# Kernel optimization log

Hardware: AMD Instinct MI355X
Metric: run time of the kernel (lower is better)

## Reference

```python
import jax, jax.numpy as jnp
import numpy as np

N_NODES = 50000
D_IN = 128
HIDDEN = 128
UNITS_DENSE = 256
N_EDGES = 600000
N_PRED = 200000
N_SEL = 300000


def setup_inputs() -> dict:
    key = jax.random.key(0)
    ks = jax.random.split(key, 12)
    node_state = jax.random.normal(ks[0], (N_NODES, D_IN), jnp.float32)
    edge_index = jax.random.randint(ks[1], (2, N_EDGES), 0, N_NODES, jnp.int32)
    out_edges = jax.random.randint(ks[2], (2, N_PRED), 0, N_NODES, jnp.int32)
    set_idx = jnp.sort(jax.random.randint(ks[3], (N_SEL,), 0, 2 * N_PRED, jnp.int32))
    # Glorot-ish scaled weights
    W1 = jax.random.normal(ks[4], (D_IN, HIDDEN), jnp.float32) / np.float32(np.sqrt(D_IN))
    b1 = jnp.zeros((HIDDEN,), jnp.float32)
    W2 = jax.random.normal(ks[5], (HIDDEN, HIDDEN), jnp.float32) / np.float32(np.sqrt(HIDDEN))
    b2 = jnp.zeros((HIDDEN,), jnp.float32)
    dense_W = jax.random.normal(ks[6], (2 * 0 + HIDDEN, UNITS_DENSE), jnp.float32) / np.float32(np.sqrt(HIDDEN))
    dense_b = jnp.zeros((UNITS_DENSE,), jnp.float32)
    out_W = jax.random.normal(ks[7], (UNITS_DENSE, 2), jnp.float32) / np.float32(np.sqrt(UNITS_DENSE))
    out_b = jnp.zeros((2,), jnp.float32)
    return {
        "node_state": node_state, "edge_index": edge_index, "out_edges": out_edges,
        "set_idx": set_idx, "W1": W1, "b1": b1, "W2": W2, "b2": b2,
        "dense_W": dense_W, "dense_b": dense_b, "out_W": out_W, "out_b": out_b,
    }


def _graph_conv(h, src, dst, W, b):
    """DGL GraphConv, norm='both', no activation: D_in^{-1/2} A D_out^{-1/2} H W + b."""
    n = h.shape[0]
    ones = jnp.ones(src.shape[0], h.dtype)
    deg_out = jnp.clip(jax.ops.segment_sum(ones, src, num_segments=n), 1.0)  # [N]
    deg_in = jnp.clip(jax.ops.segment_sum(ones, dst, num_segments=n), 1.0)   # [N]
    h = (h * jax.lax.rsqrt(deg_out)[:, None]) @ W                            # [N, H]
    agg = jax.ops.segment_sum(h[src], dst, num_segments=n)                   # [N, H]
    return agg * jax.lax.rsqrt(deg_in)[:, None] + b


def reference(node_state, edge_index, out_edges, set_idx,
              W1, b1, W2, b2, dense_W, dense_b, out_W, out_b):
    src, dst = edge_index[0], edge_index[1]
    h = _graph_conv(node_state, src, dst, W1, b1)
    h = _graph_conv(h, src, dst, W2, b2)
    # concat along axis=0 as in the original: [2*E_pred, H]
    edge_state = jnp.concatenate([h[out_edges[0]], h[out_edges[1]]], axis=0)
    # boolean_mask replaced by equivalent gather of selected (True) rows
    edge_state_set = edge_state[set_idx]                                      # [N_SEL, H]
    hidden = jax.nn.relu(edge_state_set @ dense_W + dense_b)
    return jax.nn.softmax(hidden @ out_W + out_b, axis=-1)
```

## Files before the change

kernel.cpp:

```cpp
#include <hip/hip_runtime.h>

#define NN 50000
#define DD 128
#define NE 600000
#define NP 200000
#define NS 300000
#define NU 256
#define NBH 64
#define EPB 9375
#define NW 12500
#define NB64 782

typedef __attribute__((ext_vector_type(8))) short short8;
typedef __attribute__((ext_vector_type(4))) float floatx4;

__device__ inline float bf2f(unsigned int u16) {
    unsigned int x = u16 << 16;
    float f; __builtin_memcpy(&f, &x, 4); return f;
}
__device__ inline unsigned short f2bf(float f) {
    unsigned int x; __builtin_memcpy(&x, &f, 4);
    unsigned int lsb = (x >> 16) & 1u;
    x += 0x7fffu + lsb;
    return (unsigned short)(x >> 16);
}

__global__ __launch_bounds__(256) void k_hist(const int* __restrict__ ei,
                                              unsigned int* __restrict__ P) {
    __shared__ unsigned int hw[NW];
    int b = blockIdx.x, half = blockIdx.y, tid = threadIdx.x;
    for (int w = tid; w < NW; w += 256) hw[w] = 0;
    __syncthreads();
    const int* src = ei + (size_t)half * NE;
    int e0 = b * EPB, e1 = min(e0 + EPB, NE);
    for (int e = e0 + tid; e < e1; e += 256) {
        int s = src[e];
        atomicAdd(&hw[s >> 2], 1u << ((s & 3) * 8));
    }
    __syncthreads();
    unsigned int* Pb = P + ((size_t)half * NBH + b) * NW;
    for (int w = tid; w < NW; w += 256) Pb[w] = hw[w];
}

__global__ void k_reduce(const unsigned int* __restrict__ P, int* __restrict__ deg_in,
                         float* __restrict__ r) {
    int w = blockIdx.x * 256 + threadIdx.x;
    if (w >= 2 * NW) return;
    int half = (w >= NW);
    int wl = w - half * NW;
    const unsigned int* Ph = P + (size_t)half * NBH * NW + wl;
    int c0 = 0, c1 = 0, c2 = 0, c3 = 0;
    for (int b = 0; b < NBH; ++b) {
        unsigned int v = Ph[(size_t)b * NW];
        c0 += v & 0xff; c1 += (v >> 8) & 0xff; c2 += (v >> 16) & 0xff; c3 += v >> 24;
    }
    int nb = wl * 4;
    if (half) {
        int4 d = {c0, c1, c2, c3};
        *(int4*)(deg_in + nb) = d;
    }
    float4 rr = {rsqrtf((float)max(c0, 1)), rsqrtf((float)max(c1, 1)),
                 rsqrtf((float)max(c2, 1)), rsqrtf((float)max(c3, 1))};
    *(float4*)(r + (size_t)half * NN + nb) = rr;
}

__global__ __launch_bounds__(1024) void k_scan(const int* __restrict__ deg_in,
                                               int* __restrict__ row_ptr) {
    __shared__ int wsum[16];
    __shared__ int woff[16];
    __shared__ int carry_s;
    __shared__ int total_s;
    int tid = threadIdx.x, lane = tid & 63, w = tid >> 6;
    if (tid == 0) carry_s = 0;
    __syncthreads();
    for (int wb = 0; wb < NW; wb += 1024) {
        int i4 = wb + tid;
        int4 v = {0, 0, 0, 0};
        if (i4 < NW) v = *(const int4*)(deg_in + i4 * 4);
        int t0 = v.x, t1 = t0 + v.y, t2 = t1 + v.z, tot = t2 + v.w;
        int x = tot;
#pragma unroll
        for (int off = 1; off < 64; off <<= 1) {
            int y = __shfl_up(x, off);
            if (lane >= off) x += y;
        }
        if (lane == 63) wsum[w] = x;
        __syncthreads();
        if (w == 0 && lane < 16) {
            int s = wsum[lane];
            int xs = s;
#pragma unroll
            for (int off = 1; off < 16; off <<= 1) {
                int y = __shfl_up(xs, off);
                if (lane >= off) xs += y;
            }
            woff[lane] = xs - s;
            if (lane == 15) total_s = xs;
        }
        __syncthreads();
        if (i4 < NW) {
            int base = carry_s + woff[w] + x - tot;
            int4 o = {base, base + t0, base + t1, base + t2};
            *(int4*)(row_ptr + i4 * 4) = o;
        }
        __syncthreads();
        if (tid == 0) carry_s += total_s;
        __syncthreads();
    }
    if (tid == 0) row_ptr[NN] = carry_s;
}

__global__ void k_colscan(const unsigned int* __restrict__ Pin, const int* __restrict__ row_ptr,
                          int* __restrict__ basetab) {
    int n = blockIdx.x * 256 + threadIdx.x;
    if (n >= NN) return;
    int wl = n >> 2, sh = (n & 3) * 8;
    int run = row_ptr[n];
    for (int b = 0; b < NBH; ++b) {
        basetab[(size_t)b * NN + n] = run;
        run += (Pin[(size_t)b * NW + wl] >> sh) & 0xff;
    }
}

__global__ __launch_bounds__(256) void k_bucket2(const int* __restrict__ ei,
                                                 const int* __restrict__ basetab,
                                                 int* __restrict__ col) {
    __shared__ unsigned int cw[NW];
    int b = blockIdx.x, tid = threadIdx.x;
    for (int w = tid; w < NW; w += 256) cw[w] = 0;
    __syncthreads();
    const int* bt = basetab + (size_t)b * NN;
    int e0 = b * EPB, e1 = min(e0 + EPB, NE);
    for (int e = e0 + tid; e < e1; e += 256) {
        int s = ei[e], d = ei[NE + e];
        int sh = (d & 3) * 8;
        unsigned int old = atomicAdd(&cw[d >> 2], 1u << sh);
        int local = (old >> sh) & 0xff;
        col[bt[d] + local] = s;
    }
}

__global__ void k_castW(const float* __restrict__ W1, const float* __restrict__ W2,
                        const float* __restrict__ dW, unsigned short* __restrict__ BT1,
                        unsigned short* __restrict__ BT2, unsigned short* __restrict__ BTd) {
    int t = blockIdx.x * 256 + threadIdx.x;
    if (t < 16384) {
        int r = t >> 7, c = t & 127;
        BT1[c * 128 + r] = f2bf(W1[t]);
    } else if (t < 32768) {
        int t2 = t - 16384;
        int r = t2 >> 7, c = t2 & 127;
        BT2[c * 128 + r] = f2bf(W2[t2]);
    } else if (t < 65536) {
        int t2 = t - 32768;
        int r = t2 >> 8, c = t2 & 255;
        BTd[c * 128 + r] = f2bf(dW[t2]);
    }
}

template <bool ABF>
__global__ __launch_bounds__(256) void k_gemm_bf(const void* __restrict__ Ap,
                                                 const float* __restrict__ rs,
                                                 const unsigned short* __restrict__ BT,
                                                 unsigned short* __restrict__ Cm) {
    __shared__ unsigned short As[64][136];
    __shared__ unsigned short Bs[128][136];
    int tid = threadIdx.x, lane = tid & 63, wave = tid >> 6;
    int quad = lane >> 4, l16 = lane & 15;
    int row0 = blockIdx.x * 64;

    if (ABF) {
        const unsigned short* A = (const unsigned short*)Ap;
#pragma unroll
        for (int p = 0; p < 4; ++p) {
            int fid = tid + p * 256;
            int r = fid >> 4, c = fid & 15;
            int gr = row0 + r; if (gr > NN - 1) gr = NN - 1;
            *(uint4*)&As[r][c * 8] = *(const uint4*)(A + (size_t)gr * DD + c * 8);
        }
    } else {
        const float* A = (const float*)Ap;
#pragma unroll
        for (int p = 0; p < 8; ++p) {
            int fid = tid + p * 256;
            int r = fid >> 5, c = fid & 31;
            int gr = row0 + r; if (gr > NN - 1) gr = NN - 1;
            float4 v = *(const float4*)(A + (size_t)gr * DD + c * 4);
            ushort4 u;
            u.x = f2bf(v.x); u.y = f2bf(v.y); u.z = f2bf(v.z); u.w = f2bf(v.w);
            *(ushort4*)&As[r][c * 4] = u;
        }
    }
#pragma unroll
    for (int p = 0; p < 8; ++p) {
        int fid = tid + p * 256;
        int r = fid >> 4, c = fid & 15;
        *(uint4*)&Bs[r][c * 8] = *(const uint4*)(BT + (size_t)r * DD + c * 8);
    }
    __syncthreads();

    short8 af[4];
#pragma unroll
    for (int ks = 0; ks < 4; ++ks)
        af[ks] = *(const short8*)&As[wave * 16 + l16][ks * 32 + quad * 8];
    floatx4 acc[8];
#pragma unroll
    for (int nt = 0; nt < 8; ++nt) acc[nt] = (floatx4){0.f, 0.f, 0.f, 0.f};
#pragma unroll
    for (int ks = 0; ks < 4; ++ks) {
#pragma unroll
        for (int nt = 0; nt < 8; ++nt) {
            short8 bf = *(const short8*)&Bs[nt * 16 + l16][ks * 32 + quad * 8];
            acc[nt] = __builtin_amdgcn_mfma_f32_16x16x32_bf16(af[ks], bf, acc[nt], 0, 0, 0);
        }
    }
    int rbase = row0 + wave * 16 + quad * 4;
#pragma unroll
    for (int r = 0; r < 4; ++r) {
        int gr = rbase + r;
        if (gr < NN) {
            float s = rs[gr];
#pragma unroll
            for (int nt = 0; nt < 8; ++nt)
                Cm[(size_t)gr * DD + nt * 16 + l16] = f2bf(acc[nt][r] * s);
        }
    }
}

__global__ __launch_bounds__(256) void k_aggregate(const unsigned short* __restrict__ T,
                                                   const int* __restrict__ row_ptr,
                                                   const int* __restrict__ col,
                                                   const float* __restrict__ r_in,
                                                   const float* __restrict__ b,
                                                   unsigned short* __restrict__ H) {
    int wave = threadIdx.x >> 6, lane = threadIdx.x & 63;
    int sub = lane >> 4, l16 = lane & 15;
    int node = blockIdx.x * 16 + wave * 4 + sub;
    if (node >= NN) return;
    int beg = row_ptr[node], end = row_ptr[node + 1];
    float a0 = 0.f, a1 = 0.f, a2 = 0.f, a3 = 0.f, a4 = 0.f, a5 = 0.f, a6 = 0.f, a7 = 0.f;
    for (int base = beg; base < end; base += 16) {
        int m = end - base; if (m > 16) m = 16;
        int myidx = (l16 < m) ? col[base + l16] : 0;
        int j = 0;
        for (; j + 2 <= m; j += 2) {
            int s0 = __shfl(myidx, (sub << 4) | j);
            int s1 = __shfl(myidx, (sub << 4) | (j + 1));
            uint4 v0 = *(const uint4*)(T + (size_t)s0 * DD + l16 * 8);
            uint4 v1 = *(const uint4*)(T + (size_t)s1 * DD + l16 * 8);
            a0 += bf2f(v0.x & 0xffff) + bf2f(v1.x & 0xffff);
            a1 += bf2f(v0.x >> 16)    + bf2f(v1.x >> 16);
            a2 += bf2f(v0.y & 0xffff) + bf2f(v1.y & 0xffff);
            a3 += bf2f(v0.y >> 16)    + bf2f(v1.y >> 16);
            a4 += bf2f(v0.z & 0xffff) + bf2f(v1.z & 0xffff);
            a5 += bf2f(v0.z >> 16)    + bf2f(v1.z >> 16);
            a6 += bf2f(v0.w & 0xffff) + bf2f(v1.w & 0xffff);
            a7 += bf2f(v0.w >> 16)    + bf2f(v1.w >> 16);
        }
        if (j < m) {
            int s0 = __shfl(myidx, (sub << 4) | j);
            uint4 v0 = *(const uint4*)(T + (size_t)s0 * DD + l16 * 8);
            a0 += bf2f(v0.x & 0xffff); a1 += bf2f(v0.x >> 16);
            a2 += bf2f(v0.y & 0xffff); a3 += bf2f(v0.y >> 16);
            a4 += bf2f(v0.z & 0xffff); a5 += bf2f(v0.z >> 16);
            a6 += bf2f(v0.w & 0xffff); a7 += bf2f(v0.w >> 16);
        }
    }
    float rv = r_in[node];
    float4 bl = *(const float4*)(b + l16 * 8);
    float4 bh = *(const float4*)(b + l16 * 8 + 4);
    uint4 w;
    w.x = (unsigned int)f2bf(a0 * rv + bl.x) | ((unsigned int)f2bf(a1 * rv + bl.y) << 16);
    w.y = (unsigned int)f2bf(a2 * rv + bl.z) | ((unsigned int)f2bf(a3 * rv + bl.w) << 16);
    w.z = (unsigned int)f2bf(a4 * rv + bh.x) | ((unsigned int)f2bf(a5 * rv + bh.y) << 16);
    w.w = (unsigned int)f2bf(a6 * rv + bh.z) | ((unsigned int)f2bf(a7 * rv + bh.w) << 16);
    *(uint4*)(H + (size_t)node * DD + l16 * 8) = w;
}

__global__ __launch_bounds__(256) void k_mlp_mfma(const unsigned short* __restrict__ H2,
                                                  const unsigned short* __restrict__ BTd,
                                                  const float* __restrict__ db,
                                                  const float* __restrict__ oW,
                                                  const float* __restrict__ ob,
                                                  float* __restrict__ P) {
    __shared__ unsigned short As[64][136];
    __shared__ unsigned short Bs[128][136];
    int tid = threadIdx.x, lane = tid & 63, wave = tid >> 6;
    int quad = lane >> 4, l16 = lane & 15;
    int row0 = blockIdx.x * 64;
#pragma unroll
    for (int p = 0; p < 4; ++p) {
        int fid = tid + p * 256;
        int r = fid >> 4, c = fid & 15;
        int gr = row0 + r; if (gr > NN - 1) gr = NN - 1;
        *(uint4*)&As[r][c * 8] = *(const uint4*)(H2 + (size_t)gr * DD + c * 8);
    }
    short8 af[4];
    floatx4 acc[16];
#pragma unroll
    for (int i = 0; i < 16; ++i) acc[i] = (floatx4){0.f, 0.f, 0.f, 0.f};

    for (int ch = 0; ch < 2; ++ch) {
        __syncthreads();
#pragma unroll
        for (int p = 0; p < 8; ++p) {
            int fid = tid + p * 256;
            int r = fid >> 4, c = fid & 15;
            *(uint4*)&Bs[r][c * 8] = *(const uint4*)(BTd + (size_t)(ch * 128 + r) * DD + c * 8);
        }
        __syncthreads();
        if (ch == 0) {
#pragma unroll
            for (int ks = 0; ks < 4; ++ks)
                af[ks] = *(const short8*)&As[wave * 16 + l16][ks * 32 + quad * 8];
        }
#pragma unroll
        for (int ks = 0; ks < 4; ++ks) {
#pragma unroll
            for (int nt = 0; nt < 8; ++nt) {
                short8 bf = *(const short8*)&Bs[nt * 16 + l16][ks * 32 + quad * 8];
                acc[ch * 8 + nt] =
                    __builtin_amdgcn_mfma_f32_16x16x32_bf16(af[ks], bf, acc[ch * 8 + nt], 0, 0, 0);
            }
        }
    }
    int rbase = row0 + wave * 16 + quad * 4;
#pragma unroll
    for (int r = 0; r < 4; ++r) {
        float p0 = 0.f, p1 = 0.f;
#pragma unroll
        for (int ch = 0; ch < 2; ++ch) {
#pragma unroll
            for (int nt = 0; nt < 8; ++nt) {
                int colc = ch * 128 + nt * 16 + l16;
                float h = acc[ch * 8 + nt][r] + db[colc];
                h = fmaxf(h, 0.f);
                p0 += h * oW[2 * colc];
                p1 += h * oW[2 * colc + 1];
            }
        }
#pragma unroll
        for (int m = 8; m >= 1; m >>= 1) {
            p0 += __shfl_xor(p0, m, 16);
            p1 += __shfl_xor(p1, m, 16);
        }
        if (l16 == 0) {
            int gr = rbase + r;
            if (gr < NN) {
                float l0 = p0 + ob[0], l1 = p1 + ob[1];
                float mx = fmaxf(l0, l1);
                float e0 = __expf(l0 - mx), e1 = __expf(l1 - mx);
                float inv = 1.f / (e0 + e1);
                float2 pr = {e0 * inv, e1 * inv};
                *(float2*)(P + 2 * gr) = pr;
            }
        }
    }
}

__global__ void k_gather(const int* __restrict__ sidx, const int* __restrict__ oe,
                         const float* __restrict__ P, float* __restrict__ out) {
    int i = blockIdx.x * 256 + threadIdx.x;
    if (i >= NS) return;
    int node = oe[sidx[i]];
    float2 v = *(const float2*)(P + 2 * node);
    *(float2*)(out + 2 * i) = v;
}

extern "C" void kernel_launch(void* const* d_in, const int* in_sizes, int n_in,
                              void* d_out, int out_size, void* d_ws, size_t ws_size,
                              hipStream_t stream) {
    const float* node_state = (const float*)d_in[0];
    const int* ei   = (const int*)d_in[1];
    const int* oe   = (const int*)d_in[2];
    const int* sidx = (const int*)d_in[3];
    const float* W1 = (const float*)d_in[4];
    const float* b1 = (const float*)d_in[5];
    const float* W2 = (const float*)d_in[6];
    const float* b2 = (const float*)d_in[7];
    const float* dW = (const float*)d_in[8];
    const float* db = (const float*)d_in[9];
    const float* oW = (const float*)d_in[10];
    const float* ob = (const float*)d_in[11];
    float* out = (float*)d_out;

    char* ws = (char*)d_ws;
    size_t off = 0;
    auto carve = [&](size_t bytes) -> char* {
        char* p = ws + off;
        off = (off + bytes + 255) & ~(size_t)255;
        return p;
    };
    int*   deg_in  = (int*)carve((size_t)NN * 4);
    float* r       = (float*)carve((size_t)2 * NN * 4);
    int*   row_ptr = (int*)carve((size_t)(NN + 1) * 4);
    int*   col     = (int*)carve((size_t)NE * 4);
    unsigned int* P_hist = (unsigned int*)carve((size_t)2 * NBH * NW * 4);
    int*   basetab = (int*)carve((size_t)NBH * NN * 4);
    unsigned short* t   = (unsigned short*)carve((size_t)NN * DD * 2);
    unsigned short* h   = (unsigned short*)carve((size_t)NN * DD * 2);
    unsigned short* BT1 = (unsigned short*)carve((size_t)DD * DD * 2);
    unsigned short* BT2 = (unsigned short*)carve((size_t)DD * DD * 2);
    unsigned short* BTd = (unsigned short*)carve((size_t)DD * NU * 2);
    float* P = (float*)t;

    float* r_out = r;
    float* r_in  = r + NN;

    k_hist<<<dim3(NBH, 2), 256, 0, stream>>>(ei, P_hist);
    k_reduce<<<(2 * NW + 255) / 256, 256, 0, stream>>>(P_hist, deg_in, r);
    k_scan<<<1, 1024, 0, stream>>>(deg_in, row_ptr);
    k_colscan<<<(NN + 255) / 256, 256, 0, stream>>>(P_hist + (size_t)NBH * NW, row_ptr, basetab);
    k_bucket2<<<NBH, 256, 0, stream>>>(ei, basetab, col);

    k_castW<<<256, 256, 0, stream>>>(W1, W2, dW, BT1, BT2, BTd);

    k_gemm_bf<false><<<NB64, 256, 0, stream>>>(node_state, r_out, BT1, t);
    k_aggregate<<<(NN + 15) / 16, 256, 0, stream>>>(t, row_ptr, col, r_in, b1, h);

    k_gemm_bf<true><<<NB64, 256, 0, stream>>>(h, r_out, BT2, t);
    k_aggregate<<<(NN + 15) / 16, 256, 0, stream>>>(t, row_ptr, col, r_in, b2, h);

    k_mlp_mfma<<<NB64, 256, 0, stream>>>(h, BTd, db, oW, ob, P);
    k_gather<<<(NS + 255) / 256, 256, 0, stream>>>(sidx, oe, P, out);
}
```

Measured before the change: 266.9 us.

## Fuse CSR build and weight cast into one cooperative kernel with grid syncs

Result: slower. 416.2 us (+55.9%).

```diff
diff --git a/kernel.cpp b/kernel.cpp
--- a/kernel.cpp
+++ b/kernel.cpp
@@ -1,4 +1,7 @@
 #include <hip/hip_runtime.h>
+#include <hip/hip_cooperative_groups.h>
+
+namespace cg = cooperative_groups;
 
 #define NN 50000
 #define DD 128
@@ -6,8 +9,8 @@
 #define NP 200000
 #define NS 300000
 #define NU 256
-#define NBH 64
-#define EPB 9375
+#define NBH 128
+#define EPB 4688
 #define NW 12500
 #define NB64 782
 
@@ -25,136 +28,122 @@
     return (unsigned short)(x >> 16);
 }
 
-__global__ __launch_bounds__(256) void k_hist(const int* __restrict__ ei,
-                                              unsigned int* __restrict__ P) {
+__global__ __launch_bounds__(256) void k_csr_coop(
+    const int* __restrict__ ei,
+    const float* __restrict__ W1, const float* __restrict__ W2, const float* __restrict__ dW,
+    unsigned short* __restrict__ BT1, unsigned short* __restrict__ BT2,
+    unsigned short* __restrict__ BTd,
+    unsigned int* __restrict__ P_hist, int* __restrict__ deg_in, float* __restrict__ r,
+    int* __restrict__ row_ptr, int* __restrict__ basetab, int* __restrict__ col,
+    int* __restrict__ blocksum, int* __restrict__ blockoff)
+{
     __shared__ unsigned int hw[NW];
-    int b = blockIdx.x, half = blockIdx.y, tid = threadIdx.x;
+    cg::grid_group grid = cg::this_grid();
+    int b = blockIdx.x, tid = threadIdx.x, lane = tid & 63;
+
     for (int w = tid; w < NW; w += 256) hw[w] = 0;
     __syncthreads();
-    const int* src = ei + (size_t)half * NE;
-    int e0 = b * EPB, e1 = min(e0 + EPB, NE);
+    int chunk = b & 127;
+    const int* eptr = ei + (b < 128 ? NE : 0);
+    int e0 = chunk * EPB, e1 = min(e0 + EPB, NE);
     for (int e = e0 + tid; e < e1; e += 256) {
-        int s = src[e];
-        atomicAdd(&hw[s >> 2], 1u << ((s & 3) * 8));
+        int v = eptr[e];
+        atomicAdd(&hw[v >> 2], 1u << ((v & 3) * 8));
     }
     __syncthreads();
-    unsigned int* Pb = P + ((size_t)half * NBH + b) * NW;
-    for (int w = tid; w < NW; w += 256) Pb[w] = hw[w];
-}
-
-__global__ void k_reduce(const unsigned int* __restrict__ P, int* __restrict__ deg_in,
-                         float* __restrict__ r) {
-    int w = blockIdx.x * 256 + threadIdx.x;
-    if (w >= 2 * NW) return;
-    int half = (w >= NW);
-    int wl = w - half * NW;
-    const unsigned int* Ph = P + (size_t)half * NBH * NW + wl;
-    int c0 = 0, c1 = 0, c2 = 0, c3 = 0;
-    for (int b = 0; b < NBH; ++b) {
-        unsigned int v = Ph[(size_t)b * NW];
-        c0 += v & 0xff; c1 += (v >> 8) & 0xff; c2 += (v >> 16) & 0xff; c3 += v >> 24;
-    }
-    int nb = wl * 4;
-    if (half) {
-        int4 d = {c0, c1, c2, c3};
-        *(int4*)(deg_in + nb) = d;
-    }
-    float4 rr = {rsqrtf((float)max(c0, 1)), rsqrtf((float)max(c1, 1)),
-                 rsqrtf((float)max(c2, 1)), rsqrtf((float)max(c3, 1))};
-    *(float4*)(r + (size_t)half * NN + nb) = rr;
-}
-
-__global__ __launch_bounds__(1024) void k_scan(const int* __restrict__ deg_in,
-                                               int* __restrict__ row_ptr) {
-    __shared__ int wsum[16];
-    __shared__ int woff[16];
-    __shared__ int carry_s;
-    __shared__ int total_s;
-    int tid = threadIdx.x, lane = tid & 63, w = tid >> 6;
-    if (tid == 0) carry_s = 0;
+    {
+        unsigned int* Pb = P_hist + (size_t)b * NW;
+        for (int w = tid; w < NW; w += 256) Pb[w] = hw[w];
+    }
+    grid.sync();
+
+    int gid = b * 256 + tid;
+    if (gid < 2 * NW) {
+        int half = gid >= NW;
+        int wl = gid - half * NW;
+        const unsigned int* Ph = P_hist + (size_t)(half ? 128 : 0) * NW + wl;
+        int c0 = 0, c1 = 0, c2 = 0, c3 = 0;
+        for (int b2 = 0; b2 < 128; ++b2) {
+            unsigned int v = Ph[(size_t)b2 * NW];
+            c0 += v & 0xff; c1 += (v >> 8) & 0xff; c2 += (v >> 16) & 0xff; c3 += v >> 24;
+        }
+        int nb4 = wl * 4;
+        if (!half) { int4 d4 = {c0, c1, c2, c3}; *(int4*)(deg_in + nb4) = d4; }
+        float4 rr = {rsqrtf((float)max(c0, 1)), rsqrtf((float)max(c1, 1)),
+                     rsqrtf((float)max(c2, 1)), rsqrtf((float)max(c3, 1))};
+        *(float4*)(r + (half ? 0 : NN) + nb4) = rr;
+    }
+    {
+        int t = gid;
+        if (t < 16384) { int rr = t >> 7, cc = t & 127; BT1[cc * 128 + rr] = f2bf(W1[t]); }
+        else if (t < 32768) { int t2 = t - 16384; int rr = t2 >> 7, cc = t2 & 127; BT2[cc * 128 + rr] = f2bf(W2[t2]); }
+        else { int t2 = t - 32768; int rr = t2 >> 8, cc = t2 & 255; BTd[cc * 128 + rr] = f2bf(dW[t2]); }
+    }
+    grid.sync();
+
+    int w49 = b * 49 + tid;
+    bool valid = (tid < 49) && (w49 < NW);
+    int4 v4 = {0, 0, 0, 0};
+    if (valid) v4 = *(const int4*)(deg_in + w49 * 4);
+    if (tid < 64) {
+        int s = v4.x + v4.y + v4.z + v4.w;
+        int x = s;
+#pragma unroll
+        for (int off = 1; off < 64; off <<= 1) { int y = __shfl_up(x, off); if (lane >= off) x += y; }
+        hw[tid] = (unsigned int)(x - s);
+        if (lane == 63) blocksum[b] = x;
+    }
+    grid.sync();
+
+    if (b == 0 && tid < 64) {
+        int s0 = blocksum[tid * 4], s1 = blocksum[tid * 4 + 1];
+        int s2 = blocksum[tid * 4 + 2], s3 = blocksum[tid * 4 + 3];
+        int tot = s0 + s1 + s2 + s3;
+        int x = tot;
+#pragma unroll
+        for (int off = 1; off < 64; off <<= 1) { int y = __shfl_up(x, off); if (lane >= off) x += y; }
+        int base0 = x - tot;
+        blockoff[tid * 4]     = base0;
+        blockoff[tid * 4 + 1] = base0 + s0;
+        blockoff[tid * 4 + 2] = base0 + s0 + s1;
+        blockoff[tid * 4 + 3] = base0 + s0 + s1 + s2;
+    }
+    grid.sync();
+
+    int bo = blockoff[b];
+    if (valid) {
+        int base = bo + (int)hw[tid];
+        int4 o = {base, base + v4.x, base + v4.x + v4.y, base + v4.x + v4.y + v4.z};
+        *(int4*)(row_ptr + w49 * 4) = o;
+        hw[256 + tid * 4]     = (unsigned int)o.x;
+        hw[256 + tid * 4 + 1] = (unsigned int)o.y;
+        hw[256 + tid * 4 + 2] = (unsigned int)o.z;
+        hw[256 + tid * 4 + 3] = (unsigned int)o.w;
+    }
+    if (b == 0 && tid == 0) row_ptr[NN] = NE;
     __syncthreads();
-    for (int wb = 0; wb < NW; wb += 1024) {
-        int i4 = wb + tid;
-        int4 v = {0, 0, 0, 0};
-        if (i4 < NW) v = *(const int4*)(deg_in + i4 * 4);
-        int t0 = v.x, t1 = t0 + v.y, t2 = t1 + v.z, tot = t2 + v.w;
-        int x = tot;
-#pragma unroll
-        for (int off = 1; off < 64; off <<= 1) {
-            int y = __shfl_up(x, off);
-            if (lane >= off) x += y;
-        }
-        if (lane == 63) wsum[w] = x;
-        __syncthreads();
-        if (w == 0 && lane < 16) {
-            int s = wsum[lane];
-            int xs = s;
-#pragma unroll
-            for (int off = 1; off < 16; off <<= 1) {
-                int y = __shfl_up(xs, off);
-                if (lane >= off) xs += y;
-            }
-            woff[lane] = xs - s;
-            if (lane == 15) total_s = xs;
-        }
-        __syncthreads();
-        if (i4 < NW) {
-            int base = carry_s + woff[w] + x - tot;
-            int4 o = {base, base + t0, base + t1, base + t2};
-            *(int4*)(row_ptr + i4 * 4) = o;
-        }
-        __syncthreads();
-        if (tid == 0) carry_s += total_s;
-        __syncthreads();
-    }
-    if (tid == 0) row_ptr[NN] = carry_s;
-}
-
-__global__ void k_colscan(const unsigned int* __restrict__ Pin, const int* __restrict__ row_ptr,
-                          int* __restrict__ basetab) {
-    int n = blockIdx.x * 256 + threadIdx.x;
-    if (n >= NN) return;
-    int wl = n >> 2, sh = (n & 3) * 8;
-    int run = row_ptr[n];
-    for (int b = 0; b < NBH; ++b) {
-        basetab[(size_t)b * NN + n] = run;
-        run += (Pin[(size_t)b * NW + wl] >> sh) & 0xff;
-    }
-}
-
-__global__ __launch_bounds__(256) void k_bucket2(const int* __restrict__ ei,
-                                                 const int* __restrict__ basetab,
-                                                 int* __restrict__ col) {
-    __shared__ unsigned int cw[NW];
-    int b = blockIdx.x, tid = threadIdx.x;
-    for (int w = tid; w < NW; w += 256) cw[w] = 0;
+
+    int n = b * 196 + tid;
+    if (tid < 196 && n < NN) {
+        int run = (int)hw[256 + tid];
+        int wl = n >> 2, sh = (n & 3) * 8;
+        for (int b2 = 0; b2 < 128; ++b2) {
+            basetab[(size_t)b2 * NN + n] = run;
+            run += (P_hist[(size_t)b2 * NW + wl] >> sh) & 0xff;
+        }
+    }
+    grid.sync();
+
+    if (b >= 128) return;
+    for (int w = tid; w < NW; w += 256) hw[w] = 0;
     __syncthreads();
     const int* bt = basetab + (size_t)b * NN;
-    int e0 = b * EPB, e1 = min(e0 + EPB, NE);
     for (int e = e0 + tid; e < e1; e += 256) {
         int s = ei[e], d = ei[NE + e];
         int sh = (d & 3) * 8;
-        unsigned int old = atomicAdd(&cw[d >> 2], 1u << sh);
+        unsigned int old = atomicAdd(&hw[d >> 2], 1u << sh);
         int local = (old >> sh) & 0xff;
         col[bt[d] + local] = s;
-    }
-}
-
-__global__ void k_castW(const float* __restrict__ W1, const float* __restrict__ W2,
-                        const float* __restrict__ dW, unsigned short* __restrict__ BT1,
-                        unsigned short* __restrict__ BT2, unsigned short* __restrict__ BTd) {
-    int t = blockIdx.x * 256 + threadIdx.x;
-    if (t < 16384) {
-        int r = t >> 7, c = t & 127;
-        BT1[c * 128 + r] = f2bf(W1[t]);
-    } else if (t < 32768) {
-        int t2 = t - 16384;
-        int r = t2 >> 7, c = t2 & 127;
-        BT2[c * 128 + r] = f2bf(W2[t2]);
-    } else if (t < 65536) {
-        int t2 = t - 32768;
-        int r = t2 >> 8, c = t2 & 255;
-        BTd[c * 128 + r] = f2bf(dW[t2]);
     }
 }
 
@@ -243,21 +232,25 @@
         int m = end - base; if (m > 16) m = 16;
         int myidx = (l16 < m) ? col[base + l16] : 0;
         int j = 0;
-        for (; j + 2 <= m; j += 2) {
+        for (; j + 4 <= m; j += 4) {
             int s0 = __shfl(myidx, (sub << 4) | j);
             int s1 = __shfl(myidx, (sub << 4) | (j + 1));
+            int s2 = __shfl(myidx, (sub << 4) | (j + 2));
+            int s3 = __shfl(myidx, (sub << 4) | (j + 3));
             uint4 v0 = *(const uint4*)(T + (size_t)s0 * DD + l16 * 8);
             uint4 v1 = *(const uint4*)(T + (size_t)s1 * DD + l16 * 8);
-            a0 += bf2f(v0.x & 0xffff) + bf2f(v1.x & 0xffff);
-            a1 += bf2f(v0.x >> 16)    + bf2f(v1.x >> 16);
-            a2 += bf2f(v0.y & 0xffff) + bf2f(v1.y & 0xffff);
-            a3 += bf2f(v0.y >> 16)    + bf2f(v1.y >> 16);
-            a4 += bf2f(v0.z & 0xffff) + bf2f(v1.z & 0xffff);
-            a5 += bf2f(v0.z >> 16)    + bf2f(v1.z >> 16);
-            a6 += bf2f(v0.w & 0xffff) + bf2f(v1.w & 0xffff);
-            a7 += bf2f(v0.w >> 16)    + bf2f(v1.w >> 16);
-        }
-        if (j < m) {
+            uint4 v2 = *(const uint4*)(T + (size_t)s2 * DD + l16 * 8);
+            uint4 v3 = *(const uint4*)(T + (size_t)s3 * DD + l16 * 8);
+            a0 += bf2f(v0.x & 0xffff) + bf2f(v1.x & 0xffff) + bf2f(v2.x & 0xffff) + bf2f(v3.x & 0xffff);
+            a1 += bf2f(v0.x >> 16)    + bf2f(v1.x >> 16)    + bf2f(v2.x >> 16)    + bf2f(v3.x >> 16);
+            a2 += bf2f(v0.y & 0xffff) + bf2f(v1.y & 0xffff) + bf2f(v2.y & 0xffff) + bf2f(v3.y & 0xffff);
+            a3 += bf2f(v0.y >> 16)    + bf2f(v1.y >> 16)    + bf2f(v2.y >> 16)    + bf2f(v3.y >> 16);
+            a4 += bf2f(v0.z & 0xffff) + bf2f(v1.z & 0xffff) + bf2f(v2.z & 0xffff) + bf2f(v3.z & 0xffff);
+            a5 += bf2f(v0.z >> 16)    + bf2f(v1.z >> 16)    + bf2f(v2.z >> 16)    + bf2f(v3.z >> 16);
+            a6 += bf2f(v0.w & 0xffff) + bf2f(v1.w & 0xffff) + bf2f(v2.w & 0xffff) + bf2f(v3.w & 0xffff);
+            a7 += bf2f(v0.w >> 16)    + bf2f(v1.w >> 16)    + bf2f(v2.w >> 16)    + bf2f(v3.w >> 16);
+        }
+        for (; j < m; ++j) {
             int s0 = __shfl(myidx, (sub << 4) | j);
             uint4 v0 = *(const uint4*)(T + (size_t)s0 * DD + l16 * 8);
             a0 += bf2f(v0.x & 0xffff); a1 += bf2f(v0.x >> 16);
@@ -397,6 +390,8 @@
     int*   col     = (int*)carve((size_t)NE * 4);
     unsigned int* P_hist = (unsigned int*)carve((size_t)2 * NBH * NW * 4);
     int*   basetab = (int*)carve((size_t)NBH * NN * 4);
+    int*   blocksum = (int*)carve(256 * 4);
+    int*   blockoff = (int*)carve(256 * 4);
     unsigned short* t   = (unsigned short*)carve((size_t)NN * DD * 2);
     unsigned short* h   = (unsigned short*)carve((size_t)NN * DD * 2);
     unsigned short* BT1 = (unsigned short*)carve((size_t)DD * DD * 2);
@@ -407,13 +402,12 @@
     float* r_out = r;
     float* r_in  = r + NN;
 
-    k_hist<<<dim3(NBH, 2), 256, 0, stream>>>(ei, P_hist);
-    k_reduce<<<(2 * NW + 255) / 256, 256, 0, stream>>>(P_hist, deg_in, r);
-    k_scan<<<1, 1024, 0, stream>>>(deg_in, row_ptr);
-    k_colscan<<<(NN + 255) / 256, 256, 0, stream>>>(P_hist + (size_t)NBH * NW, row_ptr, basetab);
-    k_bucket2<<<NBH, 256, 0, stream>>>(ei, basetab, col);
-
-    k_castW<<<256, 256, 0, stream>>>(W1, W2, dW, BT1, BT2, BTd);
+    void* args[] = {(void*)&ei, (void*)&W1, (void*)&W2, (void*)&dW,
+                    (void*)&BT1, (void*)&BT2, (void*)&BTd,
+                    (void*)&P_hist, (void*)&deg_in, (void*)&r,
+                    (void*)&row_ptr, (void*)&basetab, (void*)&col,
+                    (void*)&blocksum, (void*)&blockoff};
+    hipLaunchCooperativeKernel((const void*)k_csr_coop, dim3(256), dim3(256), args, 0, stream);
 
     k_gemm_bf<false><<<NB64, 256, 0, stream>>>(node_state, r_out, BT1, t);
     k_aggregate<<<(NN + 15) / 16, 256, 0, stream>>>(t, row_ptr, col, r_in, b1, h);
```
